# Kernel tuning notes

Hardware: AMD Instinct MI355X
Metric: run time of the kernel (lower is better)

The kernel has to match this reference:

```python
import jax, jax.numpy as jnp
import numpy as np
import math

H = 80; W = 80
FOVX = math.pi / 2.0; FOVY = math.pi / 2.0
TANX = math.tan(FOVX * 0.5); TANY = math.tan(FOVY * 0.5)
FOCAL_X = W / (2.0 * TANX); FOCAL_Y = H / (2.0 * TANY)
SCALE_MOD = 1.0
N_GAUSS = 4096; K_GEOM = 1024; K_SH = 1024

SH_C0 = 0.28209479177387814
SH_C1 = 0.4886025119029199
C2 = [1.0925484305920792, -1.0925484305920792, 0.31539156525252005, -1.0925484305920792, 0.5462742152960396]
C3 = [-0.5900435899266435, 2.890611442640554, -0.4570457994644658, 0.3731763325901154, -0.4570457994644658, 1.445305721320277, -0.5900435899266435]


def eval_sh3(sh, d):
    # sh: [N,16,3], d: [N,3] unit view directions -> clamped RGB [N,3]
    x, y, z = d[:, 0:1], d[:, 1:2], d[:, 2:3]
    xx, yy, zz = x * x, y * y, z * z
    xy, yz, xz = x * y, y * z, x * z
    res = (SH_C0 * sh[:, 0]
           - SH_C1 * y * sh[:, 1] + SH_C1 * z * sh[:, 2] - SH_C1 * x * sh[:, 3]
           + C2[0] * xy * sh[:, 4] + C2[1] * yz * sh[:, 5]
           + C2[2] * (2.0 * zz - xx - yy) * sh[:, 6]
           + C2[3] * xz * sh[:, 7] + C2[4] * (xx - yy) * sh[:, 8]
           + C3[0] * y * (3.0 * xx - yy) * sh[:, 9] + C3[1] * xy * z * sh[:, 10]
           + C3[2] * y * (4.0 * zz - xx - yy) * sh[:, 11]
           + C3[3] * z * (2.0 * zz - 3.0 * xx - 3.0 * yy) * sh[:, 12]
           + C3[4] * x * (4.0 * zz - xx - yy) * sh[:, 13]
           + C3[5] * z * (xx - yy) * sh[:, 14]
           + C3[6] * x * (xx - yy - 3.0 * zz) * sh[:, 15])
    return jnp.maximum(res + 0.5, 0.0)


def quat_to_rotmat(q):
    # q: [N,4] normalized (w,x,y,z) -> [N,3,3]
    w, x, y, z = q[:, 0], q[:, 1], q[:, 2], q[:, 3]
    r0 = jnp.stack([1 - 2 * (y * y + z * z), 2 * (x * y - w * z), 2 * (x * z + w * y)], -1)
    r1 = jnp.stack([2 * (x * y + w * z), 1 - 2 * (x * x + z * z), 2 * (y * z - w * x)], -1)
    r2 = jnp.stack([2 * (x * z - w * y), 2 * (y * z + w * x), 1 - 2 * (x * x + y * y)], -1)
    return jnp.stack([r0, r1, r2], axis=1)


def _forward(means3D, sh, sh_indices, g_indices, opacities, scales, scale_factors, rotations, extrinsic, bg):
    N = means3D.shape[0]
    # row-vector convention as in the torch wrapper: p_hom = [x,y,z,1] @ view
    R3 = extrinsic[:3, :3]; t3 = extrinsic[3, :3]
    p_view = means3D @ R3 + t3  # [N,3] camera space
    tx, ty, tz = p_view[:, 0], p_view[:, 1], p_view[:, 2]
    in_front = tz > 0.2  # near-plane cull as in CUDA kernel
    tz_s = jnp.where(in_front, tz, 1.0)
    # NDC (projection matrix reduces to x/(z tanx), y/(z tany)) then ndc2Pix
    gx = ((tx / (tz_s * TANX) + 1.0) * W - 1.0) * 0.5
    gy = ((ty / (tz_s * TANY) + 1.0) * H - 1.0) * 0.5
    # indexed 3D covariance: Sigma = R diag(s^2) R^T, codebook gathers
    s = scales[g_indices] * scale_factors * SCALE_MOD  # [N,3]
    q = rotations[g_indices]
    q = q / jnp.linalg.norm(q, axis=1, keepdims=True)
    Rm = quat_to_rotmat(q)
    cov3D = jnp.einsum('nij,nj,nkj->nik', Rm, s * s, Rm)
    # EWA splat: world->cam rotation is R3^T under row-vector storage
    Wm = R3.T
    cov_cam = jnp.einsum('ij,njk,lk->nil', Wm, cov3D, Wm)
    limx = 1.3 * TANX; limy = 1.3 * TANY
    txc = jnp.clip(tx / tz_s, -limx, limx) * tz_s
    tyc = jnp.clip(ty / tz_s, -limy, limy) * tz_s
    J = jnp.zeros((N, 2, 3), means3D.dtype)
    J = J.at[:, 0, 0].set(FOCAL_X / tz_s).at[:, 0, 2].set(-FOCAL_X * txc / (tz_s * tz_s))
    J = J.at[:, 1, 1].set(FOCAL_Y / tz_s).at[:, 1, 2].set(-FOCAL_Y * tyc / (tz_s * tz_s))
    cov2d = jnp.einsum('nij,njk,nlk->nil', J, cov_cam, J)
    a = cov2d[:, 0, 0] + 0.3; b = cov2d[:, 0, 1]; c = cov2d[:, 1, 1] + 0.3
    det = a * c - b * b
    valid = in_front & (det > 0)
    det_s = jnp.where(det != 0, det, 1.0)
    ca = c / det_s; cb = -b / det_s; cc = a / det_s  # conic
    mid = 0.5 * (a + c)
    lam1 = mid + jnp.sqrt(jnp.maximum(0.1, mid * mid - det))
    radii = jnp.where(valid, jnp.ceil(3.0 * jnp.sqrt(lam1)), 0.0).astype(jnp.int32)
    # SH -> RGB, view dir from camera position (extrinsic.inverse()[3,:3])
    campos = jnp.linalg.inv(extrinsic)[3, :3]
    dirs = means3D - campos
    dirs = dirs / jnp.linalg.norm(dirs, axis=1, keepdims=True)
    color = eval_sh3(sh[sh_indices], dirs)  # [N,3]
    # global front-to-back depth sort
    depth = jnp.where(valid, tz, jnp.inf)
    order = jnp.argsort(depth)
    gx_s, gy_s = gx[order], gy[order]
    ca_s, cb_s, cc_s = ca[order], cb[order], cc[order]
    op_s = opacities[order, 0]; col_s = color[order]; val_s = valid[order]
    # pixel grid (pixel centers at integer coords as in renderCUDA)
    ys, xs = jnp.meshgrid(jnp.arange(H, dtype=means3D.dtype), jnp.arange(W, dtype=means3D.dtype), indexing='ij')
    px = xs.reshape(-1); py = ys.reshape(-1)  # [P]
    dx = gx_s[None, :] - px[:, None]  # [P,N]
    dy = gy_s[None, :] - py[:, None]
    power = -0.5 * (ca_s * dx * dx + cc_s * dy * dy) - cb_s * dx * dy
    alpha = jnp.minimum(0.99, op_s[None, :] * jnp.exp(jnp.minimum(power, 0.0)))
    keep = (power <= 0.0) & val_s[None, :] & (alpha >= 1.0 / 255.0)
    alpha = jnp.where(keep, alpha, 0.0)
    om = 1.0 - alpha
    T_inc = jnp.cumprod(om, axis=1)
    inc = T_inc >= 1e-4  # early-termination prefix (T monotone)
    T_excl = jnp.concatenate([jnp.ones((px.shape[0], 1), om.dtype), T_inc[:, :-1]], axis=1)
    w = alpha * T_excl * inc
    T_final = jnp.prod(jnp.where(inc, om, 1.0), axis=1)
    out = w @ col_s + T_final[:, None] * bg[None, :]  # [P,3]
    color_img = jnp.transpose(out.reshape(H, W, 3), (2, 0, 1))  # [3,H,W]
    return color_img, radii


def setup_inputs() -> dict:
    key = jax.random.key(0)
    ks = jax.random.split(key, 9)
    xy = (jax.random.uniform(ks[0], (N_GAUSS, 2)) - 0.5) * 4.0
    z = jax.random.uniform(ks[1], (N_GAUSS, 1)) * 4.0 + 2.0
    means3D = jnp.concatenate([xy, z], axis=1)  # inside the view frustum
    sh = jax.random.normal(ks[2], (K_SH, 16, 3)) * 0.3
    sh_indices = jax.random.randint(ks[3], (N_GAUSS,), 0, K_SH)
    g_indices = jax.random.randint(ks[4], (N_GAUSS,), 0, K_GEOM)
    opacities = jax.random.uniform(ks[5], (N_GAUSS, 1), minval=0.1, maxval=0.99)
    scales = jax.random.uniform(ks[6], (K_GEOM, 3), minval=0.01, maxval=0.08)
    scale_factors = jax.random.uniform(ks[7], (N_GAUSS, 1), minval=0.5, maxval=1.5)
    rotations = jax.random.normal(ks[8], (K_GEOM, 4))
    extrinsic = jnp.eye(4, dtype=jnp.float32)
    bg = jnp.zeros((3,), jnp.float32)
    return dict(means3D=means3D, sh=sh, sh_indices=sh_indices, g_indices=g_indices,
                opacities=opacities, scales=scales, scale_factors=scale_factors,
                rotations=rotations, extrinsic=extrinsic, bg=bg)


def reference(means3D, sh, sh_indices, g_indices, opacities, scales, scale_factors, rotations, extrinsic, bg):
    return _forward(means3D, sh, sh_indices, g_indices, opacities, scales, scale_factors, rotations, extrinsic, bg)
```

## Files before the change

### kernel.cpp

```cpp
#include <hip/hip_runtime.h>
#include <math.h>

#define NG 4096
#define WI 80
#define HI 80
#define NPIX (WI*HI)
#define FOCAL 40.0f
#define LIM 1.3f
#define CAP 1024

#define SH_C0 0.28209479177387814f
#define SH_C1 0.4886025119029199f

__global__ __launch_bounds__(256) void prep_k(
    const float* __restrict__ means, const float* __restrict__ sh,
    const int* __restrict__ shidx, const int* __restrict__ gidx,
    const float* __restrict__ opac, const float* __restrict__ scales,
    const float* __restrict__ sfac, const float* __restrict__ rots,
    const float* __restrict__ ext, float4* __restrict__ ws,
    float* __restrict__ radii_out)
{
  int i = blockIdx.x*blockDim.x + threadIdx.x;
  if (i >= NG) return;
  float e0=ext[0],  e1=ext[1],  e2=ext[2];
  float e4=ext[4],  e5=ext[5],  e6=ext[6];
  float e8=ext[8],  e9=ext[9],  e10=ext[10];
  float e12=ext[12], e13=ext[13], e14=ext[14];
  float m0=means[3*i+0], m1=means[3*i+1], m2=means[3*i+2];
  float tx = m0*e0 + m1*e4 + m2*e8  + e12;
  float ty = m0*e1 + m1*e5 + m2*e9  + e13;
  float tz = m0*e2 + m1*e6 + m2*e10 + e14;
  bool infront = tz > 0.2f;
  float tzs = infront ? tz : 1.0f;
  float inv_tzs = 1.0f / tzs;
  float gx = ((tx*inv_tzs + 1.0f)*WI - 1.0f)*0.5f;
  float gy = ((ty*inv_tzs + 1.0f)*HI - 1.0f)*0.5f;

  int gi = gidx[i];
  float sf = sfac[i];
  float s0 = scales[3*gi+0]*sf, s1 = scales[3*gi+1]*sf, s2 = scales[3*gi+2]*sf;
  float qw = rots[4*gi+0], qx = rots[4*gi+1], qy = rots[4*gi+2], qz = rots[4*gi+3];
  float qinv = rsqrtf(qw*qw+qx*qx+qy*qy+qz*qz);
  qw*=qinv; qx*=qinv; qy*=qinv; qz*=qinv;
  float r00 = 1.0f - 2.0f*(qy*qy+qz*qz);
  float r01 = 2.0f*(qx*qy - qw*qz);
  float r02 = 2.0f*(qx*qz + qw*qy);
  float r10 = 2.0f*(qx*qy + qw*qz);
  float r11 = 1.0f - 2.0f*(qx*qx+qz*qz);
  float r12 = 2.0f*(qy*qz - qw*qx);
  float r20 = 2.0f*(qx*qz - qw*qy);
  float r21 = 2.0f*(qy*qz + qw*qx);
  float r22 = 1.0f - 2.0f*(qx*qx+qy*qy);
  float v0 = s0*s0, v1 = s1*s1, v2 = s2*s2;
  float C00 = r00*r00*v0 + r01*r01*v1 + r02*r02*v2;
  float C01 = r00*r10*v0 + r01*r11*v1 + r02*r12*v2;
  float C02 = r00*r20*v0 + r01*r21*v1 + r02*r22*v2;
  float C11 = r10*r10*v0 + r11*r11*v1 + r12*r12*v2;
  float C12 = r10*r20*v0 + r11*r21*v1 + r12*r22*v2;
  float C22 = r20*r20*v0 + r21*r21*v1 + r22*r22*v2;
  float W0x=e0, W0y=e4, W0z=e8;
  float W1x=e1, W1y=e5, W1z=e9;
  float W2x=e2, W2y=e6, W2z=e10;
  float B00 = W0x*C00 + W0y*C01 + W0z*C02;
  float B01 = W0x*C01 + W0y*C11 + W0z*C12;
  float B02 = W0x*C02 + W0y*C12 + W0z*C22;
  float B10 = W1x*C00 + W1y*C01 + W1z*C02;
  float B11 = W1x*C01 + W1y*C11 + W1z*C12;
  float B12 = W1x*C02 + W1y*C12 + W1z*C22;
  float B20 = W2x*C00 + W2y*C01 + W2z*C02;
  float B21 = W2x*C01 + W2y*C11 + W2z*C12;
  float B22 = W2x*C02 + W2y*C12 + W2z*C22;
  float V00 = B00*W0x + B01*W0y + B02*W0z;
  float V01 = B00*W1x + B01*W1y + B02*W1z;
  float V02 = B00*W2x + B01*W2y + B02*W2z;
  float V11 = B10*W1x + B11*W1y + B12*W1z;
  float V12 = B10*W2x + B11*W2y + B12*W2z;
  float V22 = B20*W2x + B21*W2y + B22*W2z;
  float txz = tx*inv_tzs, tyz = ty*inv_tzs;
  float txc = fminf(fmaxf(txz, -LIM), LIM) * tzs;
  float tyc = fminf(fmaxf(tyz, -LIM), LIM) * tzs;
  float jx  = FOCAL*inv_tzs;
  float jy  = FOCAL*inv_tzs;
  float jz0 = -FOCAL*txc*inv_tzs*inv_tzs;
  float jz1 = -FOCAL*tyc*inv_tzs*inv_tzs;
  float c00 = jx*jx*V00 + 2.0f*jx*jz0*V02 + jz0*jz0*V22;
  float c01 = jx*jy*V01 + jx*jz1*V02 + jz0*jy*V12 + jz0*jz1*V22;
  float c11 = jy*jy*V11 + 2.0f*jy*jz1*V12 + jz1*jz1*V22;
  float a = c00 + 0.3f;
  float b = c01;
  float cf = c11 + 0.3f;
  float det = a*cf - b*b;
  bool valid = infront && (det > 0.0f);
  float dets = (det != 0.0f) ? det : 1.0f;
  float ca = cf/dets, cb = -b/dets, cc = a/dets;
  float mid = 0.5f*(a+cf);
  float lam1 = mid + sqrtf(fmaxf(0.1f, mid*mid - det));
  float radf = valid ? ceilf(3.0f*sqrtf(lam1)) : 0.0f;
  radii_out[i] = radf;

  float op = valid ? opac[i] : 0.0f;
  float L2 = 2.0f*fmaxf(0.0f, logf(255.0f*op));
  float rcx = valid ? sqrtf(L2*a)  + 0.01f : 0.0f;
  float rcy = valid ? sqrtf(L2*cf) + 0.01f : 0.0f;

  float cp0 = -(e12*e0 + e13*e1 + e14*e2);
  float cp1 = -(e12*e4 + e13*e5 + e14*e6);
  float cp2 = -(e12*e8 + e13*e9 + e14*e10);
  float dx0 = m0-cp0, dy0 = m1-cp1, dz0 = m2-cp2;
  float dn = rsqrtf(dx0*dx0+dy0*dy0+dz0*dz0);
  float x = dx0*dn, y = dy0*dn, z = dz0*dn;
  float xx=x*x, yy=y*y, zz=z*z;
  float xy=x*y, yz=y*z, xz=x*z;
  float bf[16];
  bf[0]  = SH_C0;
  bf[1]  = -SH_C1*y;
  bf[2]  =  SH_C1*z;
  bf[3]  = -SH_C1*x;
  bf[4]  =  1.0925484305920792f*xy;
  bf[5]  = -1.0925484305920792f*yz;
  bf[6]  =  0.31539156525252005f*(2.0f*zz-xx-yy);
  bf[7]  = -1.0925484305920792f*xz;
  bf[8]  =  0.5462742152960396f*(xx-yy);
  bf[9]  = -0.5900435899266435f*y*(3.0f*xx-yy);
  bf[10] =  2.890611442640554f*xy*z;
  bf[11] = -0.4570457994644658f*y*(4.0f*zz-xx-yy);
  bf[12] =  0.3731763325901154f*z*(2.0f*zz-3.0f*xx-3.0f*yy);
  bf[13] = -0.4570457994644658f*x*(4.0f*zz-xx-yy);
  bf[14] =  1.445305721320277f*z*(xx-yy);
  bf[15] = -0.5900435899266435f*x*(xx-yy-3.0f*zz);
  const float* S = sh + (long)shidx[i]*48;
  float cr=0.f, cg=0.f, cbl=0.f;
  #pragma unroll
  for (int j=0;j<16;j++) {
    float w = bf[j];
    cr  += w*S[j*3+0];
    cg  += w*S[j*3+1];
    cbl += w*S[j*3+2];
  }
  cr  = fmaxf(cr +0.5f, 0.0f);
  cg  = fmaxf(cg +0.5f, 0.0f);
  cbl = fmaxf(cbl+0.5f, 0.0f);

  ws[i]        = make_float4(gx, gy, rcx, rcy);
  ws[NG + i]   = make_float4(ca, cb, cc, op);
  ws[2*NG + i] = make_float4(cr, cg, cbl, infront ? tz : __builtin_inff());
}

__global__ __launch_bounds__(512) void tile_k(const float4* __restrict__ ws,
                                              const float* __restrict__ bg,
                                              float* __restrict__ out)
{
  __shared__ unsigned long long kds[CAP];
  __shared__ int    sidx[CAP];
  __shared__ float2 sgxy[CAP];
  __shared__ float4 sabc[CAP];
  __shared__ float4 scol[CAP];
  __shared__ float pT[8][64], pR[8][64], pG[8][64], pB[8][64];
  __shared__ int scnt;
  int tid = threadIdx.x;
  int wv = tid >> 6, lane = tid & 63;
  if (tid == 0) scnt = 0;
  __syncthreads();

  int tile = blockIdx.x;
  int x0 = (tile % 10) * 8, y0 = (tile / 10) * 8;
  float bx0 = (float)x0, bx1 = (float)(x0+7);
  float by0 = (float)y0, by1 = (float)(y0+7);

  const float* wsf = (const float*)ws;
  for (int c = 0; c < NG/512; ++c) {
    int g = c*512 + tid;
    float4 v = ws[g];
    bool hit = (v.z > 0.0f) &&
               (v.x + v.z >= bx0) && (v.x - v.z <= bx1) &&
               (v.y + v.w >= by0) && (v.y - v.w <= by1);
    unsigned long long m = __ballot(hit);
    if (m) {
      int wcnt = __popcll(m);
      int base = 0;
      if (lane == 0) base = atomicAdd(&scnt, wcnt);
      base = __shfl(base, 0, 64);
      if (hit) {
        int pos = base + __popcll(m & ((1ull<<lane)-1ull));
        if (pos < CAP) {
          float depth = wsf[(2*NG + g)*4 + 3];
          kds[pos] = ((unsigned long long)__float_as_uint(depth) << 32) | (unsigned)g;
        }
      }
    }
  }
  __syncthreads();
  int cnt = scnt; if (cnt > CAP) cnt = CAP;

  for (int i = tid; i < cnt; i += 512) {
    unsigned long long ki = kds[i];
    int r = 0;
    #pragma unroll 8
    for (int j = 0; j < cnt; ++j) r += (kds[j] < ki);
    sidx[r] = (int)(ki & 0xFFFFFFFFull);
  }
  __syncthreads();

  for (int i = tid; i < cnt; i += 512) {
    int g = sidx[i];
    float4 v = ws[g];
    sgxy[i] = make_float2(v.x, v.y);
    sabc[i] = ws[NG + g];
    scol[i] = ws[2*NG + g];
  }
  __syncthreads();

  float px = (float)(x0 + (lane & 7));
  float py = (float)(y0 + (lane >> 3));
  int seg = (cnt + 7) >> 3;
  int s0i = wv*seg;
  int s1i = s0i + seg; if (s1i > cnt) s1i = cnt;
  float T = 1.0f, ar = 0.f, ag = 0.f, ab = 0.f;
  for (int e0 = s0i; e0 < s1i && __ballot(T >= 1e-4f); e0 += 16) {
    int e1 = e0 + 16; if (e1 > s1i) e1 = s1i;
    #pragma unroll 4
    for (int e = e0; e < e1; ++e) {
      float2 xyv = sgxy[e];
      float4 q   = sabc[e];
      float dx = xyv.x - px, dy = xyv.y - py;
      float power = -0.5f*(q.x*dx*dx + q.z*dy*dy) - q.y*dx*dy;
      float al = 0.0f;
      if (power <= 0.0f) {
        float av = fminf(0.99f, q.w*__expf(power));
        if (av >= (1.0f/255.0f)) al = av;
      }
      float4 cl = scol[e];
      float w = al*T;
      ar += w*cl.x; ag += w*cl.y; ab += w*cl.z;
      T *= 1.0f - al;
    }
  }
  pT[wv][lane]=T; pR[wv][lane]=ar; pG[wv][lane]=ag; pB[wv][lane]=ab;
  __syncthreads();

  if (tid < 64) {
    float Tg = 1.0f, r = 0.f, g2 = 0.f, b2 = 0.f;
    #pragma unroll
    for (int w = 0; w < 8; ++w) {
      r  += Tg*pR[w][tid];
      g2 += Tg*pG[w][tid];
      b2 += Tg*pB[w][tid];
      Tg *= pT[w][tid];
    }
    int p = (y0 + (tid>>3))*WI + (x0 + (tid&7));
    out[0*NPIX+p] = r  + Tg*bg[0];
    out[1*NPIX+p] = g2 + Tg*bg[1];
    out[2*NPIX+p] = b2 + Tg*bg[2];
  }
}

extern "C" void kernel_launch(void* const* d_in, const int* in_sizes, int n_in,
                              void* d_out, int out_size, void* d_ws, size_t ws_size,
                              hipStream_t stream) {
  const float* means  = (const float*)d_in[0];
  const float* sh     = (const float*)d_in[1];
  const int*   shidx  = (const int*)  d_in[2];
  const int*   gidx   = (const int*)  d_in[3];
  const float* opac   = (const float*)d_in[4];
  const float* scales = (const float*)d_in[5];
  const float* sfac   = (const float*)d_in[6];
  const float* rots   = (const float*)d_in[7];
  const float* ext    = (const float*)d_in[8];
  const float* bg     = (const float*)d_in[9];
  float* out = (float*)d_out;
  float4* ws = (float4*)d_ws;

  prep_k<<<NG/256, 256, 0, stream>>>(means, sh, shidx, gidx, opac, scales, sfac,
                                     rots, ext, ws, out + 3*NPIX);
  tile_k<<<100, 512, 0, stream>>>(ws, bg, out);
}
```

Measured before the change: 93.86 us.

## Globally depth-sort gaussians once and order-preserving tile binning

Replaces the per-tile O(cnt^2) rank sort in shared memory with one global rank sort of all gaussians: a rank kernel counts, across a 2D grid, how many keys are smaller than each key and accumulates with atomics, then a scatter kernel writes the data in depth order. Tile binning then only needs an order-preserving prefix compaction over waves, which gives sorted per-tile lists directly. Rasterization reads gaussian data from global memory through shuffled indices instead of staging it in LDS. This adds two kernel launches, global atomics and per-iteration block syncs in binning, plus gathered global loads in the inner loop, in exchange for removing the quadratic per-tile sort.

```diff
diff --git a/kernel.cpp b/kernel.cpp
--- a/kernel.cpp
+++ b/kernel.cpp
@@ -7,17 +7,27 @@
 #define NPIX (WI*HI)
 #define FOCAL 40.0f
 #define LIM 1.3f
-#define CAP 1024
+#define CAP 1536
 
 #define SH_C0 0.28209479177387814f
 #define SH_C1 0.4886025119029199f
+
+#define U0_OFF 0
+#define U1_OFF (64*1024)
+#define U2_OFF (128*1024)
+#define S0_OFF (192*1024)
+#define B1_OFF (256*1024)
+#define B2_OFF (320*1024)
+#define B3_OFF (384*1024)
+#define KD_OFF (400*1024)
+#define RK_OFF (432*1024)
 
 __global__ __launch_bounds__(256) void prep_k(
     const float* __restrict__ means, const float* __restrict__ sh,
     const int* __restrict__ shidx, const int* __restrict__ gidx,
     const float* __restrict__ opac, const float* __restrict__ scales,
     const float* __restrict__ sfac, const float* __restrict__ rots,
-    const float* __restrict__ ext, float4* __restrict__ ws,
+    const float* __restrict__ ext, char* __restrict__ wsb,
     float* __restrict__ radii_out)
 {
   int i = blockIdx.x*blockDim.x + threadIdx.x;
@@ -71,8 +81,8 @@
   float B21 = W2x*C01 + W2y*C11 + W2z*C12;
   float B22 = W2x*C02 + W2y*C12 + W2z*C22;
   float V00 = B00*W0x + B01*W0y + B02*W0z;
+  float V02 = B00*W2x + B01*W2y + B02*W2z;
   float V01 = B00*W1x + B01*W1y + B02*W1z;
-  float V02 = B00*W2x + B01*W2y + B02*W2z;
   float V11 = B10*W1x + B11*W1y + B12*W1z;
   float V12 = B10*W2x + B11*W2y + B12*W2z;
   float V22 = B20*W2x + B21*W2y + B22*W2z;
@@ -141,74 +151,90 @@
   cg  = fmaxf(cg +0.5f, 0.0f);
   cbl = fmaxf(cbl+0.5f, 0.0f);
 
-  ws[i]        = make_float4(gx, gy, rcx, rcy);
-  ws[NG + i]   = make_float4(ca, cb, cc, op);
-  ws[2*NG + i] = make_float4(cr, cg, cbl, infront ? tz : __builtin_inff());
-}
-
-__global__ __launch_bounds__(512) void tile_k(const float4* __restrict__ ws,
+  float depth = infront ? tz : __builtin_inff();
+  ((float4*)(wsb + U0_OFF))[i] = make_float4(gx, gy, rcx, rcy);
+  ((float4*)(wsb + U1_OFF))[i] = make_float4(ca, cb, cc, op);
+  ((float4*)(wsb + U2_OFF))[i] = make_float4(cr, cg, cbl, 0.0f);
+  ((unsigned long long*)(wsb + KD_OFF))[i] =
+      ((unsigned long long)__float_as_uint(depth) << 32) | (unsigned)i;
+  ((int*)(wsb + RK_OFF))[i] = 0;
+}
+
+__global__ __launch_bounds__(256) void rank_k(const char* __restrict__ wsb,
+                                              int* __restrict__ rank)
+{
+  const unsigned long long* kd = (const unsigned long long*)(wsb + KD_OFF);
+  int tid = threadIdx.x;
+  int i = blockIdx.x*256 + tid;
+  unsigned long long ki = kd[i];
+  int jb = blockIdx.y*256;
+  int r = 0;
+  #pragma unroll 8
+  for (int jj = 0; jj < 256; ++jj) {
+    unsigned long long kj = kd[jb + ((tid + jj) & 255)];
+    r += (kj < ki);
+  }
+  atomicAdd(&rank[i], r);
+}
+
+__global__ __launch_bounds__(256) void scatter_k(char* __restrict__ wsb)
+{
+  int i = blockIdx.x*256 + threadIdx.x;
+  int r = ((const int*)(wsb + RK_OFF))[i];
+  float4 u0 = ((const float4*)(wsb + U0_OFF))[i];
+  float4 u1 = ((const float4*)(wsb + U1_OFF))[i];
+  float4 u2 = ((const float4*)(wsb + U2_OFF))[i];
+  ((float4*)(wsb + S0_OFF))[r] = u0;
+  ((float4*)(wsb + B1_OFF))[r] = make_float4(u0.x, u0.y, u1.x, u1.y);
+  ((float4*)(wsb + B2_OFF))[r] = make_float4(u1.z, u1.w, u2.x, u2.y);
+  ((float*) (wsb + B3_OFF))[r] = u2.z;
+}
+
+__global__ __launch_bounds__(512) void tile_k(const char* __restrict__ wsb,
                                               const float* __restrict__ bg,
                                               float* __restrict__ out)
 {
-  __shared__ unsigned long long kds[CAP];
-  __shared__ int    sidx[CAP];
-  __shared__ float2 sgxy[CAP];
-  __shared__ float4 sabc[CAP];
-  __shared__ float4 scol[CAP];
+  __shared__ int sidx[CAP];
+  __shared__ int wcnt[2][8];
   __shared__ float pT[8][64], pR[8][64], pG[8][64], pB[8][64];
-  __shared__ int scnt;
+  const float4* S0 = (const float4*)(wsb + S0_OFF);
+  const float4* B1 = (const float4*)(wsb + B1_OFF);
+  const float4* B2 = (const float4*)(wsb + B2_OFF);
+  const float*  B3 = (const float*) (wsb + B3_OFF);
+
   int tid = threadIdx.x;
   int wv = tid >> 6, lane = tid & 63;
-  if (tid == 0) scnt = 0;
-  __syncthreads();
-
   int tile = blockIdx.x;
   int x0 = (tile % 10) * 8, y0 = (tile / 10) * 8;
   float bx0 = (float)x0, bx1 = (float)(x0+7);
   float by0 = (float)y0, by1 = (float)(y0+7);
 
-  const float* wsf = (const float*)ws;
+  int scnt = 0;
   for (int c = 0; c < NG/512; ++c) {
-    int g = c*512 + tid;
-    float4 v = ws[g];
+    int i = c*512 + tid;
+    float4 v = S0[i];
     bool hit = (v.z > 0.0f) &&
                (v.x + v.z >= bx0) && (v.x - v.z <= bx1) &&
                (v.y + v.w >= by0) && (v.y - v.w <= by1);
     unsigned long long m = __ballot(hit);
-    if (m) {
-      int wcnt = __popcll(m);
-      int base = 0;
-      if (lane == 0) base = atomicAdd(&scnt, wcnt);
-      base = __shfl(base, 0, 64);
-      if (hit) {
-        int pos = base + __popcll(m & ((1ull<<lane)-1ull));
-        if (pos < CAP) {
-          float depth = wsf[(2*NG + g)*4 + 3];
-          kds[pos] = ((unsigned long long)__float_as_uint(depth) << 32) | (unsigned)g;
-        }
-      }
+    int par = c & 1;
+    if (lane == 0) wcnt[par][wv] = __popcll(m);
+    __syncthreads();
+    int pre = 0, tot = 0;
+    #pragma unroll
+    for (int w = 0; w < 8; ++w) {
+      int cw = wcnt[par][w];
+      pre += (w < wv) ? cw : 0;
+      tot += cw;
     }
+    if (hit) {
+      int pos = scnt + pre + __popcll(m & ((1ull<<lane)-1ull));
+      if (pos < CAP) sidx[pos] = i;
+    }
+    scnt += tot;
   }
   __syncthreads();
   int cnt = scnt; if (cnt > CAP) cnt = CAP;
-
-  for (int i = tid; i < cnt; i += 512) {
-    unsigned long long ki = kds[i];
-    int r = 0;
-    #pragma unroll 8
-    for (int j = 0; j < cnt; ++j) r += (kds[j] < ki);
-    sidx[r] = (int)(ki & 0xFFFFFFFFull);
-  }
-  __syncthreads();
-
-  for (int i = tid; i < cnt; i += 512) {
-    int g = sidx[i];
-    float4 v = ws[g];
-    sgxy[i] = make_float2(v.x, v.y);
-    sabc[i] = ws[NG + g];
-    scol[i] = ws[2*NG + g];
-  }
-  __syncthreads();
 
   float px = (float)(x0 + (lane & 7));
   float py = (float)(y0 + (lane >> 3));
@@ -216,23 +242,28 @@
   int s0i = wv*seg;
   int s1i = s0i + seg; if (s1i > cnt) s1i = cnt;
   float T = 1.0f, ar = 0.f, ag = 0.f, ab = 0.f;
-  for (int e0 = s0i; e0 < s1i && __ballot(T >= 1e-4f); e0 += 16) {
-    int e1 = e0 + 16; if (e1 > s1i) e1 = s1i;
-    #pragma unroll 4
-    for (int e = e0; e < e1; ++e) {
-      float2 xyv = sgxy[e];
-      float4 q   = sabc[e];
-      float dx = xyv.x - px, dy = xyv.y - py;
-      float power = -0.5f*(q.x*dx*dx + q.z*dy*dy) - q.y*dx*dy;
-      float al = 0.0f;
-      if (power <= 0.0f) {
-        float av = fminf(0.99f, q.w*__expf(power));
-        if (av >= (1.0f/255.0f)) al = av;
+  for (int eb = s0i; eb < s1i; eb += 64) {
+    int nn = s1i - eb; if (nn > 64) nn = 64;
+    int myidx = (lane < nn) ? sidx[eb + lane] : 0;
+    for (int c16 = 0; c16 < nn && __ballot(T >= 1e-4f); c16 += 16) {
+      int ce = c16 + 16; if (ce > nn) ce = nn;
+      #pragma unroll 4
+      for (int e = c16; e < ce; ++e) {
+        int g = __shfl(myidx, e, 64);
+        float4 q1 = B1[g];
+        float4 q2 = B2[g];
+        float  b3 = B3[g];
+        float dx = q1.x - px, dy = q1.y - py;
+        float power = -0.5f*(q1.z*dx*dx + q2.x*dy*dy) - q1.w*dx*dy;
+        float al = 0.0f;
+        if (power <= 0.0f) {
+          float av = fminf(0.99f, q2.y*__expf(power));
+          if (av >= (1.0f/255.0f)) al = av;
+        }
+        float w = al*T;
+        ar += w*q2.z; ag += w*q2.w; ab += w*b3;
+        T *= 1.0f - al;
       }
-      float4 cl = scol[e];
-      float w = al*T;
-      ar += w*cl.x; ag += w*cl.y; ab += w*cl.z;
-      T *= 1.0f - al;
     }
   }
   pT[wv][lane]=T; pR[wv][lane]=ar; pG[wv][lane]=ag; pB[wv][lane]=ab;
@@ -268,9 +299,12 @@
   const float* ext    = (const float*)d_in[8];
   const float* bg     = (const float*)d_in[9];
   float* out = (float*)d_out;
-  float4* ws = (float4*)d_ws;
+  char* wsb = (char*)d_ws;
 
   prep_k<<<NG/256, 256, 0, stream>>>(means, sh, shidx, gidx, opac, scales, sfac,
-                                     rots, ext, ws, out + 3*NPIX);
-  tile_k<<<100, 512, 0, stream>>>(ws, bg, out);
-}
+                                     rots, ext, wsb, out + 3*NPIX);
+  dim3 rg(NG/256, NG/256);
+  rank_k<<<rg, 256, 0, stream>>>(wsb, (int*)(wsb + RK_OFF));
+  scatter_k<<<NG/256, 256, 0, stream>>>(wsb);
+  tile_k<<<100, 512, 0, stream>>>(wsb, bg, out);
+}
```

New measurement: 115.2 us. 1.23x slower.
